# Kernel optimization log

Measured on AMD Instinct MI355X. Metric: run time of the kernel, lower is better.

The kernel has to match this reference:

```python
import jax, jax.numpy as jnp
import numpy as np

B, N, D = 8, 2048, 1024  # batch, seq_len, input_dim (= dim_k = dim_v)

def setup_inputs() -> dict:
    key = jax.random.key(0)
    k1, k2, k3, k4, k5 = jax.random.split(key, 5)
    s = 1.0 / np.sqrt(D)
    return {
        "img": jax.random.normal(k1, (B, N, D), dtype=jnp.float32),
        "text": jax.random.normal(k2, (B, N, D), dtype=jnp.float32),
        "Wq": jax.random.normal(k3, (D, D), dtype=jnp.float32) * s,
        "Wk": jax.random.normal(k4, (D, D), dtype=jnp.float32) * s,
        "Wv": jax.random.normal(k5, (D, D), dtype=jnp.float32) * s,
    }

def reference(img, text, Wq, Wk, Wv):
    # Linear layers (bias=False): y = x @ W^T (torch Linear convention)
    Q = jnp.einsum('bnd,kd->bnk', img, Wq)    # [B, N, dim_k]
    K = jnp.einsum('bmd,kd->bmk', text, Wk)   # [B, M, dim_k]
    V = jnp.einsum('bmd,vd->bmv', text, Wv)   # [B, M, dim_v]
    alpha_qk = jnp.einsum('bnk,bmk->bnm', Q, K)  # QK^T, no 1/sqrt(dk) scaling (as in source)
    alpha = jax.nn.softmax(alpha_qk, axis=1)     # softmax over QUERY axis (dim=1), as in source
    out = jnp.einsum('bnm,bmv->bnv', alpha, V)   # [B, N, dim_v]
    feature = out + text
    return (out, feature)
```

## Files before the change

### kernel.cpp

```cpp
#include <hip/hip_runtime.h>
#include <math.h>

#define B 8
#define N 2048
#define D 1024

#define BM 128
#define BN 128
#define BK 32

typedef __bf16 bf16;
typedef __bf16 bf16x8 __attribute__((ext_vector_type(8)));
typedef __bf16 bf16x4 __attribute__((ext_vector_type(4)));
typedef float f32x4 __attribute__((ext_vector_type(4)));

__device__ __forceinline__ void load_lds16(const void* g, void* l) {
    __builtin_amdgcn_global_load_lds((const __attribute__((address_space(1))) void*)g,
                                     (__attribute__((address_space(3))) void*)l, 16, 0, 0);
}

#define MFMA16(a, b, c) __builtin_amdgcn_mfma_f32_16x16x32_bf16(a, b, c, 0, 0, 0)
#define BARRIER() asm volatile("s_barrier" ::: "memory")
#define WAITV0() asm volatile("s_waitcnt vmcnt(0)" ::: "memory")

__global__ __launch_bounds__(256) void split_fp32(const float* __restrict__ x,
                                                  bf16* __restrict__ h,
                                                  bf16* __restrict__ l, long n)
{
    long i = ((long)blockIdx.x * 256 + threadIdx.x) * 4;
    if (i >= n) return;
    float4 v = *(const float4*)(x + i);
    float vs[4] = {v.x, v.y, v.z, v.w};
    bf16x4 hh, ll;
#pragma unroll
    for (int t = 0; t < 4; ++t) {
        bf16 hv = (bf16)vs[t];
        hh[t] = hv;
        ll[t] = (bf16)(vs[t] - (float)hv);
    }
    *(bf16x4*)(h + i) = hh;
    *(bf16x4*)(l + i) = ll;
}

__global__ __launch_bounds__(256) void tsplit_1024(const float* __restrict__ W,
                                                   bf16* __restrict__ WT_h,
                                                   bf16* __restrict__ WT_l)
{
    __shared__ float tile[64][65];
    const int d0 = blockIdx.x * 64, k0 = blockIdx.y * 64;
    const int tx = threadIdx.x & 63, ty = threadIdx.x >> 6;
#pragma unroll
    for (int r = 0; r < 16; ++r) {
        int kl = ty + r * 4;
        tile[kl][tx] = W[(size_t)(k0 + kl) * 1024 + d0 + tx];
    }
    __syncthreads();
#pragma unroll
    for (int r = 0; r < 16; ++r) {
        int dl = ty + r * 4;
        float v = tile[tx][dl];
        bf16 hv = (bf16)v;
        size_t idx = (size_t)(d0 + dl) * 1024 + k0 + tx;
        WT_h[idx] = hv;
        WT_l[idx] = (bf16)(v - (float)hv);
    }
}

template<int TERMS, int EPI>
__global__ __launch_bounds__(256) void gemm_nt_mfma(
    const bf16* __restrict__ Ah_g, const bf16* __restrict__ Al_g,
    const bf16* __restrict__ Bh_g, const bf16* __restrict__ Bl_g,
    bf16* __restrict__ Chi, bf16* __restrict__ Clo,
    float* __restrict__ Cf, const float* __restrict__ Text,
    float* __restrict__ Feat,
    int Mdim, int Ncdim, int Kdim, long sA, long sB, long sC)
{
    __shared__ bf16 Ah[BM][BK];
    __shared__ bf16 Bh[BN][BK];
    __shared__ bf16 Al[BM][BK];
    __shared__ bf16 Bl[BN][BK];

    const int tid = threadIdx.x;
    const int lane = tid & 63;
    const int wv = tid >> 6;
    const int wr = (wv >> 1) * 64;
    const int wc = (wv & 1) * 64;
    const int mfrag = lane & 15;
    const int quad = lane >> 4;

    const long z = blockIdx.z;
    const int row0 = blockIdx.y * BM;
    const int col0 = blockIdx.x * BN;

    const bf16* Abh = Ah_g + z * sA;
    const bf16* Abl = (TERMS == 3) ? (Al_g + z * sA) : nullptr;
    const bf16* Bbh = Bh_g + z * sB;
    const bf16* Bbl = (TERMS == 3) ? (Bl_g + z * sB) : nullptr;

    f32x4 acc[4][4] = {};

    for (int k0 = 0; k0 < Kdim; k0 += BK) {
#pragma unroll
        for (int q = 0; q < 2; ++q) {
            int c = q * 256 + tid;
            int row = c >> 2, kp = (c & 3) * 8;
            load_lds16(Abh + (long)(row0 + row) * Kdim + k0 + kp, &Ah[row][kp]);
            load_lds16(Bbh + (long)(col0 + row) * Kdim + k0 + kp, &Bh[row][kp]);
            if constexpr (TERMS == 3) {
                load_lds16(Abl + (long)(row0 + row) * Kdim + k0 + kp, &Al[row][kp]);
                load_lds16(Bbl + (long)(col0 + row) * Kdim + k0 + kp, &Bl[row][kp]);
            }
        }
        __syncthreads();

        bf16x8 a_h[4], b_h[4], a_l[4], b_l[4];
#pragma unroll
        for (int i = 0; i < 4; ++i) {
            a_h[i] = *(const bf16x8*)&Ah[wr + i * 16 + mfrag][quad * 8];
            b_h[i] = *(const bf16x8*)&Bh[wc + i * 16 + mfrag][quad * 8];
            if constexpr (TERMS == 3) {
                a_l[i] = *(const bf16x8*)&Al[wr + i * 16 + mfrag][quad * 8];
                b_l[i] = *(const bf16x8*)&Bl[wc + i * 16 + mfrag][quad * 8];
            }
        }
#pragma unroll
        for (int i = 0; i < 4; ++i)
#pragma unroll
            for (int j = 0; j < 4; ++j) {
                acc[i][j] = MFMA16(a_h[i], b_h[j], acc[i][j]);
                if constexpr (TERMS == 3) {
                    acc[i][j] = MFMA16(a_h[i], b_l[j], acc[i][j]);
                    acc[i][j] = MFMA16(a_l[i], b_h[j], acc[i][j]);
                }
            }
        __syncthreads();
    }

    const long cbase = z * sC;
    const bool wlo = (Clo != nullptr);
#pragma unroll
    for (int i = 0; i < 4; ++i) {
#pragma unroll
        for (int r = 0; r < 4; ++r) {
            int row = row0 + wr + i * 16 + quad * 4 + r;
#pragma unroll
            for (int j = 0; j < 4; ++j) {
                int col = col0 + wc + j * 16 + mfrag;
                long idx = cbase + (long)row * Ncdim + col;
                float v = acc[i][j][r];
                if constexpr (EPI == 0) {
                    bf16 h = (bf16)v;
                    Chi[idx] = h;
                    if (wlo) Clo[idx] = (bf16)(v - (float)h);
                } else if constexpr (EPI == 1) {
                    Cf[idx] = v;
                } else {
                    Cf[idx] = v;
                    Feat[idx] = v + Text[idx];
                }
            }
        }
    }
}


__device__ __forceinline__ void xcd_swz(int& bx, int& by, int gx, int gy) {
    int nwg = gx * gy;
    int flat = by * gx + bx;
    flat = (flat & 7) * (nwg >> 3) + (flat >> 3);
    bx = flat % gx;
    by = flat / gx;
}

__device__ __forceinline__ void stage32(const bf16* __restrict__ g, int Kd, int k0,
                                        bf16* l, int tid)
{
#pragma unroll
    for (int c = 0; c < 2; ++c) {
        int idx = c * 512 + tid;
        int row = idx >> 2;
        int slot = idx & 3;
        int kk = ((slot ^ ((row >> 1) & 3)) << 3);
        load_lds16(g + (long)row * Kd + k0 + kk, l + (size_t)idx * 8);
    }
}

__device__ __forceinline__ void stage64(const bf16* __restrict__ g, int Kd, int k0,
                                        bf16* l, int tid)
{
#pragma unroll
    for (int c = 0; c < 4; ++c) {
        int idx = c * 512 + tid;
        int row = idx >> 3;
        int slot = idx & 7;
        int kk = ((slot ^ (row & 7)) << 3);
        load_lds16(g + (long)row * Kd + k0 + kk, l + (size_t)idx * 8);
    }
}

__device__ __forceinline__ bf16x8 rd32(const bf16* l, int row, int quad) {
    return *(const bf16x8*)(l + row * 32 + ((quad ^ ((row >> 1) & 3)) << 3));
}
__device__ __forceinline__ bf16x8 rd64(const bf16* l, int row, int ks, int quad) {
    return *(const bf16x8*)(l + row * 64 + (((ks * 4 + quad) ^ (row & 7)) << 3));
}

template<int EPI>
__global__ __launch_bounds__(512) void gemm256_3t(
    const bf16* __restrict__ Ah_g, const bf16* __restrict__ Al_g,
    const bf16* __restrict__ Bh_g, const bf16* __restrict__ Bl_g,
    bf16* __restrict__ Chi, bf16* __restrict__ Clo, float* __restrict__ Cf,
    int Ncdim, int Kdim, long sA, long sB, long sC)
{
    __shared__ __align__(16) bf16 lds[2][4][256 * 32];

    const int tid = threadIdx.x;
    const int lane = tid & 63;
    const int wv = tid >> 6;
    const int wrow = (wv >> 2) << 7;
    const int wcol = (wv & 3) << 6;
    const int mfrag = lane & 15;
    const int quad = lane >> 4;

    const long z = blockIdx.z;
    int bx = blockIdx.x, by = blockIdx.y;
    xcd_swz(bx, by, gridDim.x, gridDim.y);
    const int row0 = by * 256;
    const int col0 = bx * 256;

    const bf16* Abh = Ah_g + z * sA + (long)row0 * Kdim;
    const bf16* Abl = Al_g + z * sA + (long)row0 * Kdim;
    const bf16* Bbh = Bh_g + z * sB + (long)col0 * Kdim;
    const bf16* Bbl = Bl_g + z * sB + (long)col0 * Kdim;

    f32x4 acc[8][4] = {};
    const int NT = Kdim >> 5;

    stage32(Abh, Kdim, 0, lds[0][0], tid);
    stage32(Bbh, Kdim, 0, lds[0][2], tid);
    stage32(Abl, Kdim, 0, lds[0][1], tid);
    stage32(Bbl, Kdim, 0, lds[0][3], tid);

    for (int t = 0; t < NT; ++t) {
        const int cur = t & 1;
        const bf16* LAh = lds[cur][0];
        const bf16* LAl = lds[cur][1];
        const bf16* LBh = lds[cur][2];
        const bf16* LBl = lds[cur][3];
        const bool pf = (t + 1 < NT);
        const int kn = (t + 1) << 5;

        WAITV0();
        BARRIER();

        bf16x8 ah[8], bh[4], bl[4], al[8];
#pragma unroll
        for (int i = 0; i < 8; ++i) ah[i] = rd32(LAh, wrow + i * 16 + mfrag, quad);
#pragma unroll
        for (int j = 0; j < 4; ++j) bh[j] = rd32(LBh, wcol + j * 16 + mfrag, quad);

        __builtin_amdgcn_s_setprio(1);
#pragma unroll
        for (int i = 0; i < 4; ++i)
#pragma unroll
            for (int j = 0; j < 4; ++j)
                acc[i][j] = MFMA16(ah[i], bh[j], acc[i][j]);
        __builtin_amdgcn_s_setprio(0);

        if (pf) { stage32(Abh, Kdim, kn, lds[cur ^ 1][0], tid);
                  stage32(Bbh, Kdim, kn, lds[cur ^ 1][2], tid); }

#pragma unroll
        for (int j = 0; j < 4; ++j) bl[j] = rd32(LBl, wcol + j * 16 + mfrag, quad);

        __builtin_amdgcn_s_setprio(1);
#pragma unroll
        for (int i = 4; i < 8; ++i)
#pragma unroll
            for (int j = 0; j < 4; ++j)
                acc[i][j] = MFMA16(ah[i], bh[j], acc[i][j]);
        __builtin_amdgcn_s_setprio(0);

#pragma unroll
        for (int i = 0; i < 4; ++i) al[i] = rd32(LAl, wrow + i * 16 + mfrag, quad);

        __builtin_amdgcn_s_setprio(1);
#pragma unroll
        for (int i = 0; i < 4; ++i)
#pragma unroll
            for (int j = 0; j < 4; ++j)
                acc[i][j] = MFMA16(ah[i], bl[j], acc[i][j]);
        __builtin_amdgcn_s_setprio(0);

        if (pf) { stage32(Abl, Kdim, kn, lds[cur ^ 1][1], tid);
                  stage32(Bbl, Kdim, kn, lds[cur ^ 1][3], tid); }

#pragma unroll
        for (int i = 4; i < 8; ++i) al[i] = rd32(LAl, wrow + i * 16 + mfrag, quad);

        __builtin_amdgcn_s_setprio(1);
#pragma unroll
        for (int i = 4; i < 8; ++i)
#pragma unroll
            for (int j = 0; j < 4; ++j)
                acc[i][j] = MFMA16(ah[i], bl[j], acc[i][j]);

#pragma unroll
        for (int i = 0; i < 8; ++i)
#pragma unroll
            for (int j = 0; j < 4; ++j)
                acc[i][j] = MFMA16(al[i], bh[j], acc[i][j]);
        __builtin_amdgcn_s_setprio(0);
    }

    const long cbase = z * sC;
    const bool wlo = (Clo != nullptr);
#pragma unroll
    for (int i = 0; i < 8; ++i) {
#pragma unroll
        for (int r = 0; r < 4; ++r) {
            int row = row0 + wrow + i * 16 + quad * 4 + r;
            long rbase = cbase + (long)row * Ncdim;
#pragma unroll
            for (int j = 0; j < 4; ++j) {
                int col = col0 + wcol + j * 16 + mfrag;
                float v = acc[i][j][r];
                if constexpr (EPI == 0) {
                    bf16 h = (bf16)v;
                    Chi[rbase + col] = h;
                    if (wlo) Clo[rbase + col] = (bf16)(v - (float)h);
                } else {
                    Cf[rbase + col] = v;
                }
            }
        }
    }
}

template<int EPI>
__global__ __launch_bounds__(512) void gemm256_1t(
    const bf16* __restrict__ A_g, const bf16* __restrict__ B_g,
    bf16* __restrict__ Chi, float* __restrict__ Cf,
    const float* __restrict__ Text, float* __restrict__ Feat,
    int Ncdim, int Kdim, long sA, long sB, long sC)
{
    __shared__ __align__(16) bf16 lds[2][2][256 * 64];

    const int tid = threadIdx.x;
    const int lane = tid & 63;
    const int wv = tid >> 6;
    const int wrow = (wv >> 2) << 7;
    const int wcol = (wv & 3) << 6;
    const int mfrag = lane & 15;
    const int quad = lane >> 4;

    const long z = blockIdx.z;
    int bx = blockIdx.x, by = blockIdx.y;
    xcd_swz(bx, by, gridDim.x, gridDim.y);
    const int row0 = by * 256;
    const int col0 = bx * 256;

    const bf16* Ab = A_g + z * sA + (long)row0 * Kdim;
    const bf16* Bb = B_g + z * sB + (long)col0 * Kdim;

    f32x4 acc[8][4] = {};
    const int NT = Kdim >> 6;

    stage64(Ab, Kdim, 0, lds[0][0], tid);
    stage64(Bb, Kdim, 0, lds[0][1], tid);

    for (int t = 0; t < NT; ++t) {
        const int cur = t & 1;
        const bf16* LA = lds[cur][0];
        const bf16* LB = lds[cur][1];
        const bool pf = (t + 1 < NT);
        const int kn = (t + 1) << 6;

        WAITV0();
        BARRIER();

        bf16x8 a[8][2], b[4][2];
#pragma unroll
        for (int i = 0; i < 4; ++i)
#pragma unroll
            for (int ks = 0; ks < 2; ++ks)
                a[i][ks] = rd64(LA, wrow + i * 16 + mfrag, ks, quad);
#pragma unroll
        for (int j = 0; j < 2; ++j)
#pragma unroll
            for (int ks = 0; ks < 2; ++ks)
                b[j][ks] = rd64(LB, wcol + j * 16 + mfrag, ks, quad);

        __builtin_amdgcn_s_setprio(1);
#pragma unroll
        for (int i = 0; i < 4; ++i)
#pragma unroll
            for (int j = 0; j < 2; ++j)
#pragma unroll
                for (int ks = 0; ks < 2; ++ks)
                    acc[i][j] = MFMA16(a[i][ks], b[j][ks], acc[i][j]);
        __builtin_amdgcn_s_setprio(0);

        if (pf) stage64(Ab, Kdim, kn, lds[cur ^ 1][0], tid);

#pragma unroll
        for (int j = 2; j < 4; ++j)
#pragma unroll
            for (int ks = 0; ks < 2; ++ks)
                b[j][ks] = rd64(LB, wcol + j * 16 + mfrag, ks, quad);

        __builtin_amdgcn_s_setprio(1);
#pragma unroll
        for (int i = 0; i < 4; ++i)
#pragma unroll
            for (int j = 2; j < 4; ++j)
#pragma unroll
                for (int ks = 0; ks < 2; ++ks)
                    acc[i][j] = MFMA16(a[i][ks], b[j][ks], acc[i][j]);
        __builtin_amdgcn_s_setprio(0);

#pragma unroll
        for (int i = 4; i < 8; ++i)
#pragma unroll
            for (int ks = 0; ks < 2; ++ks)
                a[i][ks] = rd64(LA, wrow + i * 16 + mfrag, ks, quad);

        __builtin_amdgcn_s_setprio(1);
#pragma unroll
        for (int i = 4; i < 8; ++i)
#pragma unroll
            for (int j = 2; j < 4; ++j)
#pragma unroll
                for (int ks = 0; ks < 2; ++ks)
                    acc[i][j] = MFMA16(a[i][ks], b[j][ks], acc[i][j]);
        __builtin_amdgcn_s_setprio(0);

        if (pf) stage64(Bb, Kdim, kn, lds[cur ^ 1][1], tid);

        __builtin_amdgcn_s_setprio(1);
#pragma unroll
        for (int i = 4; i < 8; ++i)
#pragma unroll
            for (int j = 0; j < 2; ++j)
#pragma unroll
                for (int ks = 0; ks < 2; ++ks)
                    acc[i][j] = MFMA16(a[i][ks], b[j][ks], acc[i][j]);
        __builtin_amdgcn_s_setprio(0);
    }

    const long cbase = z * sC;
#pragma unroll
    for (int i = 0; i < 8; ++i) {
#pragma unroll
        for (int r = 0; r < 4; ++r) {
            int row = row0 + wrow + i * 16 + quad * 4 + r;
            long rbase = cbase + (long)row * Ncdim;
#pragma unroll
            for (int j = 0; j < 4; ++j) {
                int col = col0 + wcol + j * 16 + mfrag;
                float v = acc[i][j][r];
                if constexpr (EPI == 0) {
                    Chi[rbase + col] = (bf16)v;
                } else {
                    Cf[rbase + col] = v;
                    Feat[rbase + col] = v + Text[rbase + col];
                }
            }
        }
    }
}

__global__ __launch_bounds__(1024) void col_softmax_bf16(const float* __restrict__ S,
                                                         bf16* __restrict__ Aout)
{
    const int b = blockIdx.x / (N / 64);
    const int mbase = (blockIdx.x % (N / 64)) * 64;
    const int t = threadIdx.x;
    const int mloc = t & 63;
    const int slice = t >> 6;
    const int m = mbase + mloc;
    const float* Sb = S + (size_t)b * N * N;
    bf16* Ab = Aout + (size_t)b * N * N;
    const int n_lo = slice * (N / 16), n_hi = n_lo + (N / 16);

    __shared__ float red_m[16][64];
    __shared__ float red_s[16][64];

    float mx = -INFINITY, s = 0.0f;
    for (int n = n_lo; n < n_hi; n += 8) {
        float x[8];
#pragma unroll
        for (int u = 0; u < 8; ++u) x[u] = Sb[(size_t)(n + u) * N + m];
        float bm = x[0];
#pragma unroll
        for (int u = 1; u < 8; ++u) bm = fmaxf(bm, x[u]);
        float nm = fmaxf(mx, bm);
        float a = 0.0f;
#pragma unroll
        for (int u = 0; u < 8; ++u) a += __expf(x[u] - nm);
        s = s * __expf(mx - nm) + a;
        mx = nm;
    }
    red_m[slice][mloc] = mx;
    red_s[slice][mloc] = s;
    __syncthreads();

    float gm = -INFINITY;
#pragma unroll
    for (int i = 0; i < 16; ++i) gm = fmaxf(gm, red_m[i][mloc]);
    float den = 0.0f;
#pragma unroll
    for (int i = 0; i < 16; ++i) den += red_s[i][mloc] * __expf(red_m[i][mloc] - gm);
    float inv = 1.0f / den;

    for (int n = n_lo; n < n_hi; n += 8) {
        float x[8];
#pragma unroll
        for (int u = 0; u < 8; ++u) x[u] = Sb[(size_t)(n + u) * N + m];
#pragma unroll
        for (int u = 0; u < 8; ++u)
            Ab[(size_t)(n + u) * N + m] = (bf16)(__expf(x[u] - gm) * inv);
    }
}

extern "C" void kernel_launch(void* const* d_in, const int* in_sizes, int n_in,
                              void* d_out, int out_size, void* d_ws, size_t ws_size,
                              hipStream_t stream)
{
    const float* img  = (const float*)d_in[0];
    const float* text = (const float*)d_in[1];
    const float* Wq   = (const float*)d_in[2];
    const float* Wk   = (const float*)d_in[3];
    const float* Wv   = (const float*)d_in[4];

    const long E  = (long)B * N * D;
    const long W2 = (long)D * D;
    const long EN = (long)B * N * N;

    char* ws = (char*)d_ws;
    float* S     = (float*)ws;
    bf16* img_h  = (bf16*)ws;
    bf16* img_l  = img_h + E;
    bf16* WqT_h  = (bf16*)(ws + (size_t)4 * E);
    bf16* WqT_l  = WqT_h + W2;
    bf16* WkT_h  = WqT_l + W2;
    bf16* WkT_l  = WkT_h + W2;
    bf16* Wqk_h  = WkT_l + W2;
    bf16* Wqk_l  = Wqk_h + W2;
    bf16* Wv_l_s = Wqk_l + W2;
    float* out_pv = (float*)ws;

    bf16* text_h = (bf16*)(ws + (size_t)EN * 4);
    bf16* text_l = text_h + E;
    bf16* VT_h   = text_l;

    bf16* T_h  = (bf16*)d_out;
    bf16* T_l  = T_h + E;
    bf16* Wv_h = T_l + E;
    bf16* alpha = (bf16*)d_out;
    float* out  = (float*)d_out;
    float* feat = out + E;

    dim3 blk(256);
    dim3 blk5(512);

    split_fp32<<<E / 1024, blk, 0, stream>>>(img,  img_h,  img_l,  E);
    split_fp32<<<E / 1024, blk, 0, stream>>>(text, text_h, text_l, E);
    split_fp32<<<W2 / 1024, blk, 0, stream>>>(Wv, Wv_h, Wv_l_s, W2);
    tsplit_1024<<<dim3(16, 16), blk, 0, stream>>>(Wq, WqT_h, WqT_l);
    tsplit_1024<<<dim3(16, 16), blk, 0, stream>>>(Wk, WkT_h, WkT_l);

    gemm_nt_mfma<3, 0><<<dim3(8, 8, 1), blk, 0, stream>>>(
        WkT_h, WkT_l, WqT_h, WqT_l, Wqk_h, Wqk_l, nullptr, nullptr, nullptr,
        D, D, D, 0, 0, 0);

    gemm256_3t<0><<<dim3(D / 256, (B * N) / 256, 1), blk5, 0, stream>>>(
        img_h, img_l, Wqk_h, Wqk_l, T_h, T_l, nullptr,
        D, D, 0, 0, 0);

    gemm256_3t<1><<<dim3(N / 256, N / 256, B), blk5, 0, stream>>>(
        T_h, T_l, text_h, text_l, nullptr, nullptr, S,
        N, D, (long)N * D, (long)N * D, (long)N * N);

    gemm256_1t<0><<<dim3(N / 256, D / 256, B), blk5, 0, stream>>>(
        Wv_h, text_h, VT_h, nullptr, nullptr, nullptr,
        N, D, 0, (long)N * D, (long)D * N);

    col_softmax_bf16<<<dim3(B * N / 64), dim3(1024), 0, stream>>>(S, alpha);

    gemm256_1t<2><<<dim3(D / 256, N / 256, B), blk5, 0, stream>>>(
        alpha, VT_h, nullptr, out_pv, text, feat,
        D, N, (long)N * N, (long)D * N, (long)N * D);

    hipMemcpyAsync(out, out_pv, (size_t)E * 4, hipMemcpyDeviceToDevice, stream);
}
```

Before: 738.0 us.

## Switch 256x256 GEMM kernels to 32x32x16 MFMA with pointer-increment staging

Replaces the 16x16x32 bf16 MFMA tiles in both the 3-term split GEMM and the single-term GEMM with 32x32x16 MFMA tiles. This halves the MFMA instruction count and cuts LDS fragment reads per output. Global-to-LDS staging now uses precomputed swizzled offsets and pointers advanced each k-step instead of recomputing addresses. The LDS read pattern and the epilogue row mapping are rewritten to match the 32x32 accumulator layout, and the larger 16-float accumulators change register pressure and the store pattern.

```diff
diff --git a/kernel.cpp b/kernel.cpp
--- a/kernel.cpp
+++ b/kernel.cpp
@@ -13,6 +13,7 @@
 typedef __bf16 bf16x8 __attribute__((ext_vector_type(8)));
 typedef __bf16 bf16x4 __attribute__((ext_vector_type(4)));
 typedef float f32x4 __attribute__((ext_vector_type(4)));
+typedef float f32x16 __attribute__((ext_vector_type(16)));
 
 __device__ __forceinline__ void load_lds16(const void* g, void* l) {
     __builtin_amdgcn_global_load_lds((const __attribute__((address_space(1))) void*)g,
@@ -20,6 +21,7 @@
 }
 
 #define MFMA16(a, b, c) __builtin_amdgcn_mfma_f32_16x16x32_bf16(a, b, c, 0, 0, 0)
+#define MFMA32(a, b, c) __builtin_amdgcn_mfma_f32_32x32x16_bf16(a, b, c, 0, 0, 0)
 #define BARRIER() asm volatile("s_barrier" ::: "memory")
 #define WAITV0() asm volatile("s_waitcnt vmcnt(0)" ::: "memory")
 
@@ -172,39 +174,6 @@
     by = flat / gx;
 }
 
-__device__ __forceinline__ void stage32(const bf16* __restrict__ g, int Kd, int k0,
-                                        bf16* l, int tid)
-{
-#pragma unroll
-    for (int c = 0; c < 2; ++c) {
-        int idx = c * 512 + tid;
-        int row = idx >> 2;
-        int slot = idx & 3;
-        int kk = ((slot ^ ((row >> 1) & 3)) << 3);
-        load_lds16(g + (long)row * Kd + k0 + kk, l + (size_t)idx * 8);
-    }
-}
-
-__device__ __forceinline__ void stage64(const bf16* __restrict__ g, int Kd, int k0,
-                                        bf16* l, int tid)
-{
-#pragma unroll
-    for (int c = 0; c < 4; ++c) {
-        int idx = c * 512 + tid;
-        int row = idx >> 3;
-        int slot = idx & 7;
-        int kk = ((slot ^ (row & 7)) << 3);
-        load_lds16(g + (long)row * Kd + k0 + kk, l + (size_t)idx * 8);
-    }
-}
-
-__device__ __forceinline__ bf16x8 rd32(const bf16* l, int row, int quad) {
-    return *(const bf16x8*)(l + row * 32 + ((quad ^ ((row >> 1) & 3)) << 3));
-}
-__device__ __forceinline__ bf16x8 rd64(const bf16* l, int row, int ks, int quad) {
-    return *(const bf16x8*)(l + row * 64 + (((ks * 4 + quad) ^ (row & 7)) << 3));
-}
-
 template<int EPI>
 __global__ __launch_bounds__(512) void gemm256_3t(
     const bf16* __restrict__ Ah_g, const bf16* __restrict__ Al_g,
@@ -219,8 +188,9 @@
     const int wv = tid >> 6;
     const int wrow = (wv >> 2) << 7;
     const int wcol = (wv & 3) << 6;
-    const int mfrag = lane & 15;
-    const int quad = lane >> 4;
+    const int rl = lane & 31;
+    const int hi = lane >> 5;
+    const int sx = (lane >> 1) & 3;
 
     const long z = blockIdx.z;
     int bx = blockIdx.x, by = blockIdx.y;
@@ -228,18 +198,32 @@
     const int row0 = by * 256;
     const int col0 = bx * 256;
 
-    const bf16* Abh = Ah_g + z * sA + (long)row0 * Kdim;
-    const bf16* Abl = Al_g + z * sA + (long)row0 * Kdim;
-    const bf16* Bbh = Bh_g + z * sB + (long)col0 * Kdim;
-    const bf16* Bbl = Bl_g + z * sB + (long)col0 * Kdim;
-
-    f32x4 acc[8][4] = {};
+    const int sr0 = tid >> 2;
+    const long soff0 = (long)sr0 * Kdim + (((tid & 3) ^ ((sr0 >> 1) & 3)) << 3);
+    const long soff1 = soff0 + ((long)Kdim << 7);
+
+    const bf16* pAh = Ah_g + z * sA + (long)row0 * Kdim;
+    const bf16* pAl = Al_g + z * sA + (long)row0 * Kdim;
+    const bf16* pBh = Bh_g + z * sB + (long)col0 * Kdim;
+    const bf16* pBl = Bl_g + z * sB + (long)col0 * Kdim;
+
+    const int rdA0 = (wrow + rl) * 32;
+    const int rdB0 = (wcol + rl) * 32;
+    const int s0 = (hi ^ sx) << 3;
+    const int s1 = ((2 + hi) ^ sx) << 3;
+
+    f32x16 acc[4][2] = {};
     const int NT = Kdim >> 5;
 
-    stage32(Abh, Kdim, 0, lds[0][0], tid);
-    stage32(Bbh, Kdim, 0, lds[0][2], tid);
-    stage32(Abl, Kdim, 0, lds[0][1], tid);
-    stage32(Bbl, Kdim, 0, lds[0][3], tid);
+    load_lds16(pAh + soff0, &lds[0][0][tid * 8]);
+    load_lds16(pAh + soff1, &lds[0][0][4096 + tid * 8]);
+    load_lds16(pBh + soff0, &lds[0][2][tid * 8]);
+    load_lds16(pBh + soff1, &lds[0][2][4096 + tid * 8]);
+    load_lds16(pAl + soff0, &lds[0][1][tid * 8]);
+    load_lds16(pAl + soff1, &lds[0][1][4096 + tid * 8]);
+    load_lds16(pBl + soff0, &lds[0][3][tid * 8]);
+    load_lds16(pBl + soff1, &lds[0][3][4096 + tid * 8]);
+    pAh += 32; pAl += 32; pBh += 32; pBl += 32;
 
     for (int t = 0; t < NT; ++t) {
         const int cur = t & 1;
@@ -247,90 +231,137 @@
         const bf16* LAl = lds[cur][1];
         const bf16* LBh = lds[cur][2];
         const bf16* LBl = lds[cur][3];
+        bf16* SAh = lds[cur ^ 1][0];
+        bf16* SAl = lds[cur ^ 1][1];
+        bf16* SBh = lds[cur ^ 1][2];
+        bf16* SBl = lds[cur ^ 1][3];
         const bool pf = (t + 1 < NT);
-        const int kn = (t + 1) << 5;
 
         WAITV0();
         BARRIER();
 
-        bf16x8 ah[8], bh[4], bl[4], al[8];
-#pragma unroll
-        for (int i = 0; i < 8; ++i) ah[i] = rd32(LAh, wrow + i * 16 + mfrag, quad);
-#pragma unroll
-        for (int j = 0; j < 4; ++j) bh[j] = rd32(LBh, wcol + j * 16 + mfrag, quad);
+        bf16x8 ah[4][2], bh[2][2], bl[2][2], al[2][2];
+#pragma unroll
+        for (int i = 0; i < 4; ++i) {
+            ah[i][0] = *(const bf16x8*)(LAh + rdA0 + i * 1024 + s0);
+            ah[i][1] = *(const bf16x8*)(LAh + rdA0 + i * 1024 + s1);
+        }
+#pragma unroll
+        for (int j = 0; j < 2; ++j) {
+            bh[j][0] = *(const bf16x8*)(LBh + rdB0 + j * 1024 + s0);
+            bh[j][1] = *(const bf16x8*)(LBh + rdB0 + j * 1024 + s1);
+        }
 
         __builtin_amdgcn_s_setprio(1);
 #pragma unroll
-        for (int i = 0; i < 4; ++i)
-#pragma unroll
-            for (int j = 0; j < 4; ++j)
-                acc[i][j] = MFMA16(ah[i], bh[j], acc[i][j]);
+        for (int i = 0; i < 2; ++i)
+#pragma unroll
+            for (int j = 0; j < 2; ++j)
+#pragma unroll
+                for (int ks = 0; ks < 2; ++ks)
+                    acc[i][j] = MFMA32(ah[i][ks], bh[j][ks], acc[i][j]);
         __builtin_amdgcn_s_setprio(0);
 
-        if (pf) { stage32(Abh, Kdim, kn, lds[cur ^ 1][0], tid);
-                  stage32(Bbh, Kdim, kn, lds[cur ^ 1][2], tid); }
-
-#pragma unroll
-        for (int j = 0; j < 4; ++j) bl[j] = rd32(LBl, wcol + j * 16 + mfrag, quad);
+        if (pf) {
+            load_lds16(pAh + soff0, SAh + tid * 8);
+            load_lds16(pAh + soff1, SAh + 4096 + tid * 8);
+            load_lds16(pBh + soff0, SBh + tid * 8);
+            load_lds16(pBh + soff1, SBh + 4096 + tid * 8);
+        }
+
+#pragma unroll
+        for (int j = 0; j < 2; ++j) {
+            bl[j][0] = *(const bf16x8*)(LBl + rdB0 + j * 1024 + s0);
+            bl[j][1] = *(const bf16x8*)(LBl + rdB0 + j * 1024 + s1);
+        }
 
         __builtin_amdgcn_s_setprio(1);
 #pragma unroll
-        for (int i = 4; i < 8; ++i)
-#pragma unroll
-            for (int j = 0; j < 4; ++j)
-                acc[i][j] = MFMA16(ah[i], bh[j], acc[i][j]);
+        for (int i = 0; i < 2; ++i)
+#pragma unroll
+            for (int j = 0; j < 2; ++j)
+#pragma unroll
+                for (int ks = 0; ks < 2; ++ks)
+                    acc[2 + i][j] = MFMA32(ah[2 + i][ks], bh[j][ks], acc[2 + i][j]);
         __builtin_amdgcn_s_setprio(0);
 
 #pragma unroll
-        for (int i = 0; i < 4; ++i) al[i] = rd32(LAl, wrow + i * 16 + mfrag, quad);
+        for (int i = 0; i < 2; ++i) {
+            al[i][0] = *(const bf16x8*)(LAl + rdA0 + i * 1024 + s0);
+            al[i][1] = *(const bf16x8*)(LAl + rdA0 + i * 1024 + s1);
+        }
 
         __builtin_amdgcn_s_setprio(1);
 #pragma unroll
-        for (int i = 0; i < 4; ++i)
-#pragma unroll
-            for (int j = 0; j < 4; ++j)
-                acc[i][j] = MFMA16(ah[i], bl[j], acc[i][j]);
+        for (int i = 0; i < 2; ++i)
+#pragma unroll
+            for (int j = 0; j < 2; ++j)
+#pragma unroll
+                for (int ks = 0; ks < 2; ++ks)
+                    acc[i][j] = MFMA32(ah[i][ks], bl[j][ks], acc[i][j]);
         __builtin_amdgcn_s_setprio(0);
 
-        if (pf) { stage32(Abl, Kdim, kn, lds[cur ^ 1][1], tid);
-                  stage32(Bbl, Kdim, kn, lds[cur ^ 1][3], tid); }
-
-#pragma unroll
-        for (int i = 4; i < 8; ++i) al[i] = rd32(LAl, wrow + i * 16 + mfrag, quad);
+        if (pf) {
+            load_lds16(pAl + soff0, SAl + tid * 8);
+            load_lds16(pAl + soff1, SAl + 4096 + tid * 8);
+            load_lds16(pBl + soff0, SBl + tid * 8);
+            load_lds16(pBl + soff1, SBl + 4096 + tid * 8);
+        }
 
         __builtin_amdgcn_s_setprio(1);
 #pragma unroll
-        for (int i = 4; i < 8; ++i)
-#pragma unroll
-            for (int j = 0; j < 4; ++j)
-                acc[i][j] = MFMA16(ah[i], bl[j], acc[i][j]);
-
-#pragma unroll
-        for (int i = 0; i < 8; ++i)
-#pragma unroll
-            for (int j = 0; j < 4; ++j)
-                acc[i][j] = MFMA16(al[i], bh[j], acc[i][j]);
+        for (int i = 0; i < 2; ++i)
+#pragma unroll
+            for (int j = 0; j < 2; ++j)
+#pragma unroll
+                for (int ks = 0; ks < 2; ++ks)
+                    acc[i][j] = MFMA32(al[i][ks], bh[j][ks], acc[i][j]);
         __builtin_amdgcn_s_setprio(0);
+
+#pragma unroll
+        for (int i = 0; i < 2; ++i) {
+            al[i][0] = *(const bf16x8*)(LAl + rdA0 + (2 + i) * 1024 + s0);
+            al[i][1] = *(const bf16x8*)(LAl + rdA0 + (2 + i) * 1024 + s1);
+        }
+
+        __builtin_amdgcn_s_setprio(1);
+#pragma unroll
+        for (int i = 0; i < 2; ++i)
+#pragma unroll
+            for (int j = 0; j < 2; ++j)
+#pragma unroll
+                for (int ks = 0; ks < 2; ++ks)
+                    acc[2 + i][j] = MFMA32(ah[2 + i][ks], bl[j][ks], acc[2 + i][j]);
+#pragma unroll
+        for (int i = 0; i < 2; ++i)
+#pragma unroll
+            for (int j = 0; j < 2; ++j)
+#pragma unroll
+                for (int ks = 0; ks < 2; ++ks)
+                    acc[2 + i][j] = MFMA32(al[i][ks], bh[j][ks], acc[2 + i][j]);
+        __builtin_amdgcn_s_setprio(0);
+
+        pAh += 32; pAl += 32; pBh += 32; pBl += 32;
     }
 
     const long cbase = z * sC;
     const bool wlo = (Clo != nullptr);
 #pragma unroll
-    for (int i = 0; i < 8; ++i) {
-#pragma unroll
-        for (int r = 0; r < 4; ++r) {
-            int row = row0 + wrow + i * 16 + quad * 4 + r;
-            long rbase = cbase + (long)row * Ncdim;
-#pragma unroll
-            for (int j = 0; j < 4; ++j) {
-                int col = col0 + wcol + j * 16 + mfrag;
+    for (int i = 0; i < 4; ++i) {
+#pragma unroll
+        for (int j = 0; j < 2; ++j) {
+            int col = col0 + wcol + j * 32 + rl;
+#pragma unroll
+            for (int r = 0; r < 16; ++r) {
+                int row = row0 + wrow + i * 32 + (r & 3) + ((r >> 2) << 3) + (hi << 2);
+                long idx = cbase + (long)row * Ncdim + col;
                 float v = acc[i][j][r];
                 if constexpr (EPI == 0) {
                     bf16 h = (bf16)v;
-                    Chi[rbase + col] = h;
-                    if (wlo) Clo[rbase + col] = (bf16)(v - (float)h);
+                    Chi[idx] = h;
+                    if (wlo) Clo[idx] = (bf16)(v - (float)h);
                 } else {
-                    Cf[rbase + col] = v;
+                    Cf[idx] = v;
                 }
             }
         }
@@ -351,8 +382,9 @@
     const int wv = tid >> 6;
     const int wrow = (wv >> 2) << 7;
     const int wcol = (wv & 3) << 6;
-    const int mfrag = lane & 15;
-    const int quad = lane >> 4;
+    const int rl = lane & 31;
+    const int hi = lane >> 5;
+    const int sx8 = lane & 7;
 
     const long z = blockIdx.z;
     int bx = blockIdx.x, by = blockIdx.y;
@@ -360,110 +392,108 @@
     const int row0 = by * 256;
     const int col0 = bx * 256;
 
-    const bf16* Ab = A_g + z * sA + (long)row0 * Kdim;
-    const bf16* Bb = B_g + z * sB + (long)col0 * Kdim;
-
-    f32x4 acc[8][4] = {};
+    const long soffS = (long)(tid >> 3) * Kdim + ((((tid & 7) ^ ((tid >> 3) & 7))) << 3);
+    const long sstep = (long)Kdim << 6;
+
+    const bf16* pA = A_g + z * sA + (long)row0 * Kdim;
+    const bf16* pB = B_g + z * sB + (long)col0 * Kdim;
+
+    const int rdA0 = (wrow + rl) * 64;
+    const int rdB0 = (wcol + rl) * 64;
+    int sl[4];
+#pragma unroll
+    for (int ks = 0; ks < 4; ++ks) sl[ks] = ((ks * 2 + hi) ^ sx8) << 3;
+
+    f32x16 acc[4][2] = {};
     const int NT = Kdim >> 6;
 
-    stage64(Ab, Kdim, 0, lds[0][0], tid);
-    stage64(Bb, Kdim, 0, lds[0][1], tid);
+#pragma unroll
+    for (int c = 0; c < 4; ++c) {
+        load_lds16(pA + soffS + c * sstep, &lds[0][0][c * 4096 + tid * 8]);
+        load_lds16(pB + soffS + c * sstep, &lds[0][1][c * 4096 + tid * 8]);
+    }
+    pA += 64; pB += 64;
 
     for (int t = 0; t < NT; ++t) {
         const int cur = t & 1;
         const bf16* LA = lds[cur][0];
         const bf16* LB = lds[cur][1];
+        bf16* SA = lds[cur ^ 1][0];
+        bf16* SB = lds[cur ^ 1][1];
         const bool pf = (t + 1 < NT);
-        const int kn = (t + 1) << 6;
 
         WAITV0();
         BARRIER();
 
-        bf16x8 a[8][2], b[4][2];
-#pragma unroll
-        for (int i = 0; i < 4; ++i)
-#pragma unroll
-            for (int ks = 0; ks < 2; ++ks)
-                a[i][ks] = rd64(LA, wrow + i * 16 + mfrag, ks, quad);
+        bf16x8 a[2][4], b[2][4];
+#pragma unroll
+        for (int ii = 0; ii < 2; ++ii)
+#pragma unroll
+            for (int ks = 0; ks < 4; ++ks)
+                a[ii][ks] = *(const bf16x8*)(LA + rdA0 + ii * 2048 + sl[ks]);
 #pragma unroll
         for (int j = 0; j < 2; ++j)
 #pragma unroll
-            for (int ks = 0; ks < 2; ++ks)
-                b[j][ks] = rd64(LB, wcol + j * 16 + mfrag, ks, quad);
+            for (int ks = 0; ks < 4; ++ks)
+                b[j][ks] = *(const bf16x8*)(LB + rdB0 + j * 2048 + sl[ks]);
 
         __builtin_amdgcn_s_setprio(1);
 #pragma unroll
-        for (int i = 0; i < 4; ++i)
-#pragma unroll
-            for (int j = 0; j < 2; ++j)
-#pragma unroll
-                for (int ks = 0; ks < 2; ++ks)
-                    acc[i][j] = MFMA16(a[i][ks], b[j][ks], acc[i][j]);
+        for (int ii = 0; ii < 2; ++ii)
+#pragma unroll
+            for (int j = 0; j < 2; ++j)
+#pragma unroll
+                for (int ks = 0; ks < 4; ++ks)
+                    acc[ii][j] = MFMA32(a[ii][ks], b[j][ks], acc[ii][j]);
         __builtin_amdgcn_s_setprio(0);
 
-        if (pf) stage64(Ab, Kdim, kn, lds[cur ^ 1][0], tid);
-
-#pragma unroll
-        for (int j = 2; j < 4; ++j)
-#pragma unroll
-            for (int ks = 0; ks < 2; ++ks)
-                b[j][ks] = rd64(LB, wcol + j * 16 + mfrag, ks, quad);
+        if (pf) {
+#pragma unroll
+            for (int c = 0; c < 4; ++c)
+                load_lds16(pA + soffS + c * sstep, SA + c * 4096 + tid * 8);
+        }
+
+#pragma unroll
+        for (int ii = 0; ii < 2; ++ii)
+#pragma unroll
+            for (int ks = 0; ks < 4; ++ks)
+                a[ii][ks] = *(const bf16x8*)(LA + rdA0 + (2 + ii) * 2048 + sl[ks]);
 
         __builtin_amdgcn_s_setprio(1);
 #pragma unroll
-        for (int i = 0; i < 4; ++i)
-#pragma unroll
-            for (int j = 2; j < 4; ++j)
-#pragma unroll
-                for (int ks = 0; ks < 2; ++ks)
-                    acc[i][j] = MFMA16(a[i][ks], b[j][ks], acc[i][j]);
+        for (int ii = 0; ii < 2; ++ii)
+#pragma unroll
+            for (int j = 0; j < 2; ++j)
+#pragma unroll
+                for (int ks = 0; ks < 4; ++ks)
+                    acc[2 + ii][j] = MFMA32(a[ii][ks], b[j][ks], acc[2 + ii][j]);
         __builtin_amdgcn_s_setprio(0);
 
-#pragma unroll
-        for (int i = 4; i < 8; ++i)
-#pragma unroll
-            for (int ks = 0; ks < 2; ++ks)
-                a[i][ks] = rd64(LA, wrow + i * 16 + mfrag, ks, quad);
-
-        __builtin_amdgcn_s_setprio(1);
-#pragma unroll
-        for (int i = 4; i < 8; ++i)
-#pragma unroll
-            for (int j = 2; j < 4; ++j)
-#pragma unroll
-                for (int ks = 0; ks < 2; ++ks)
-                    acc[i][j] = MFMA16(a[i][ks], b[j][ks], acc[i][j]);
-        __builtin_amdgcn_s_setprio(0);
-
-        if (pf) stage64(Bb, Kdim, kn, lds[cur ^ 1][1], tid);
-
-        __builtin_amdgcn_s_setprio(1);
-#pragma unroll
-        for (int i = 4; i < 8; ++i)
-#pragma unroll
-            for (int j = 0; j < 2; ++j)
-#pragma unroll
-                for (int ks = 0; ks < 2; ++ks)
-                    acc[i][j] = MFMA16(a[i][ks], b[j][ks], acc[i][j]);
-        __builtin_amdgcn_s_setprio(0);
+        if (pf) {
+#pragma unroll
+            for (int c = 0; c < 4; ++c)
+                load_lds16(pB + soffS + c * sstep, SB + c * 4096 + tid * 8);
+        }
+
+        pA += 64; pB += 64;
     }
 
     const long cbase = z * sC;
 #pragma unroll
-    for (int i = 0; i < 8; ++i) {
-#pragma unroll
-        for (int r = 0; r < 4; ++r) {
-            int row = row0 + wrow + i * 16 + quad * 4 + r;
-            long rbase = cbase + (long)row * Ncdim;
-#pragma unroll
-            for (int j = 0; j < 4; ++j) {
-                int col = col0 + wcol + j * 16 + mfrag;
+    for (int i = 0; i < 4; ++i) {
+#pragma unroll
+        for (int j = 0; j < 2; ++j) {
+            int col = col0 + wcol + j * 32 + rl;
+#pragma unroll
+            for (int r = 0; r < 16; ++r) {
+                int row = row0 + wrow + i * 32 + (r & 3) + ((r >> 2) << 3) + (hi << 2);
+                long idx = cbase + (long)row * Ncdim + col;
                 float v = acc[i][j][r];
                 if constexpr (EPI == 0) {
-                    Chi[rbase + col] = (bf16)v;
+                    Chi[idx] = (bf16)v;
                 } else {
-                    Cf[rbase + col] = v;
-                    Feat[rbase + col] = v + Text[rbase + col];
+                    Cf[idx] = v;
+                    Feat[idx] = v + Text[idx];
                 }
             }
         }
```

Result: slower. 790.0 us (+7.0%).

## Software-pipeline 3-term GEMM, fuse split launches, use 128-tile GEMM for projection

Applied to the files above, without the earlier changes.

Restructures the bf16x3 GEMM main loop so the al*bh MFMA block of each K tile is deferred into the next iteration, using ping-pong register buffers. This lets that block overlap the next tile's LDS reads, and the wait now covers both vmcnt and lgkmcnt. The img and text fp32 splits are merged into one launch. The img@Wqk projection moves from the 256-tile kernel to the 128-tile gemm_nt_mfma kernel, which gives a larger grid. The extra live register buffers raise register pressure, and the loop unrolled by two assumes NT is even.

```diff
diff --git a/kernel.cpp b/kernel.cpp
--- a/kernel.cpp
+++ b/kernel.cpp
@@ -22,6 +22,7 @@
 #define MFMA16(a, b, c) __builtin_amdgcn_mfma_f32_16x16x32_bf16(a, b, c, 0, 0, 0)
 #define BARRIER() asm volatile("s_barrier" ::: "memory")
 #define WAITV0() asm volatile("s_waitcnt vmcnt(0)" ::: "memory")
+#define WAITALL() asm volatile("s_waitcnt vmcnt(0) lgkmcnt(0)" ::: "memory")
 
 __global__ __launch_bounds__(256) void split_fp32(const float* __restrict__ x,
                                                   bf16* __restrict__ h,
@@ -29,6 +30,30 @@
 {
     long i = ((long)blockIdx.x * 256 + threadIdx.x) * 4;
     if (i >= n) return;
+    float4 v = *(const float4*)(x + i);
+    float vs[4] = {v.x, v.y, v.z, v.w};
+    bf16x4 hh, ll;
+#pragma unroll
+    for (int t = 0; t < 4; ++t) {
+        bf16 hv = (bf16)vs[t];
+        hh[t] = hv;
+        ll[t] = (bf16)(vs[t] - (float)hv);
+    }
+    *(bf16x4*)(h + i) = hh;
+    *(bf16x4*)(l + i) = ll;
+}
+
+__global__ __launch_bounds__(256) void split_fp32_x2(
+    const float* __restrict__ x0, bf16* __restrict__ h0, bf16* __restrict__ l0,
+    const float* __restrict__ x1, bf16* __restrict__ h1, bf16* __restrict__ l1,
+    long n)
+{
+    long nb = n / 1024;
+    long bid = blockIdx.x;
+    const float* x; bf16 *h, *l;
+    if (bid < nb) { x = x0; h = h0; l = l0; }
+    else { x = x1; h = h1; l = l1; bid -= nb; }
+    long i = (bid * 256 + threadIdx.x) * 4;
     float4 v = *(const float4*)(x + i);
     float vs[4] = {v.x, v.y, v.z, v.w};
     bf16x4 hh, ll;
@@ -205,6 +230,58 @@
     return *(const bf16x8*)(l + row * 64 + (((ks * 4 + quad) ^ (row & 7)) << 3));
 }
 
+
+#define TILE_BODY(T, CUR, ALP, BHP, ALF, BHF, DOPEND)                         \
+  {                                                                           \
+    const bf16* LAh = lds[CUR][0]; const bf16* LAl = lds[CUR][1];             \
+    const bf16* LBh = lds[CUR][2]; const bf16* LBl = lds[CUR][3];             \
+    bf16* SAh = lds[CUR ^ 1][0]; bf16* SAl = lds[CUR ^ 1][1];                 \
+    bf16* SBh = lds[CUR ^ 1][2]; bf16* SBl = lds[CUR ^ 1][3];                 \
+    const bool pf = ((T) + 1 < NT);                                           \
+    const int kn = ((T) + 1) << 5;                                            \
+    WAITALL();                                                                \
+    BARRIER();                                                                \
+    _Pragma("unroll") for (int i = 0; i < 8; ++i)                             \
+        ah[i] = rd32(LAh, wrow + i * 16 + mfrag, quad);                       \
+    _Pragma("unroll") for (int j = 0; j < 4; ++j)                             \
+        BHF[j] = rd32(LBh, wcol + j * 16 + mfrag, quad);                      \
+    if (DOPEND) {                                                             \
+        __builtin_amdgcn_s_setprio(1);                                        \
+        _Pragma("unroll") for (int i = 0; i < 8; ++i)                         \
+        _Pragma("unroll") for (int j = 0; j < 4; ++j)                         \
+            acc[i][j] = MFMA16(ALP[i], BHP[j], acc[i][j]);                    \
+        __builtin_amdgcn_s_setprio(0);                                        \
+    }                                                                         \
+    if (pf) { stage32(Abh, Kdim, kn, SAh, tid);                               \
+              stage32(Bbh, Kdim, kn, SBh, tid); }                             \
+    __builtin_amdgcn_s_setprio(1);                                            \
+    _Pragma("unroll") for (int i = 0; i < 4; ++i)                             \
+    _Pragma("unroll") for (int j = 0; j < 4; ++j)                             \
+        acc[i][j] = MFMA16(ah[i], BHF[j], acc[i][j]);                         \
+    __builtin_amdgcn_s_setprio(0);                                            \
+    _Pragma("unroll") for (int j = 0; j < 4; ++j)                             \
+        bl[j] = rd32(LBl, wcol + j * 16 + mfrag, quad);                       \
+    __builtin_amdgcn_s_setprio(1);                                            \
+    _Pragma("unroll") for (int i = 4; i < 8; ++i)                             \
+    _Pragma("unroll") for (int j = 0; j < 4; ++j)                             \
+        acc[i][j] = MFMA16(ah[i], BHF[j], acc[i][j]);                         \
+    __builtin_amdgcn_s_setprio(0);                                            \
+    _Pragma("unroll") for (int i = 0; i < 8; ++i)                             \
+        ALF[i] = rd32(LAl, wrow + i * 16 + mfrag, quad);                      \
+    __builtin_amdgcn_s_setprio(1);                                            \
+    _Pragma("unroll") for (int i = 0; i < 4; ++i)                             \
+    _Pragma("unroll") for (int j = 0; j < 4; ++j)                             \
+        acc[i][j] = MFMA16(ah[i], bl[j], acc[i][j]);                          \
+    __builtin_amdgcn_s_setprio(0);                                            \
+    if (pf) { stage32(Abl, Kdim, kn, SAl, tid);                               \
+              stage32(Bbl, Kdim, kn, SBl, tid); }                             \
+    __builtin_amdgcn_s_setprio(1);                                            \
+    _Pragma("unroll") for (int i = 4; i < 8; ++i)                             \
+    _Pragma("unroll") for (int j = 0; j < 4; ++j)                             \
+        acc[i][j] = MFMA16(ah[i], bl[j], acc[i][j]);                          \
+    __builtin_amdgcn_s_setprio(0);                                            \
+  }
+
 template<int EPI>
 __global__ __launch_bounds__(512) void gemm256_3t(
     const bf16* __restrict__ Ah_g, const bf16* __restrict__ Al_g,
@@ -241,77 +318,22 @@
     stage32(Abl, Kdim, 0, lds[0][1], tid);
     stage32(Bbl, Kdim, 0, lds[0][3], tid);
 
-    for (int t = 0; t < NT; ++t) {
-        const int cur = t & 1;
-        const bf16* LAh = lds[cur][0];
-        const bf16* LAl = lds[cur][1];
-        const bf16* LBh = lds[cur][2];
-        const bf16* LBl = lds[cur][3];
-        const bool pf = (t + 1 < NT);
-        const int kn = (t + 1) << 5;
-
-        WAITV0();
-        BARRIER();
-
-        bf16x8 ah[8], bh[4], bl[4], al[8];
-#pragma unroll
-        for (int i = 0; i < 8; ++i) ah[i] = rd32(LAh, wrow + i * 16 + mfrag, quad);
-#pragma unroll
-        for (int j = 0; j < 4; ++j) bh[j] = rd32(LBh, wcol + j * 16 + mfrag, quad);
-
-        __builtin_amdgcn_s_setprio(1);
-#pragma unroll
-        for (int i = 0; i < 4; ++i)
-#pragma unroll
-            for (int j = 0; j < 4; ++j)
-                acc[i][j] = MFMA16(ah[i], bh[j], acc[i][j]);
-        __builtin_amdgcn_s_setprio(0);
-
-        if (pf) { stage32(Abh, Kdim, kn, lds[cur ^ 1][0], tid);
-                  stage32(Bbh, Kdim, kn, lds[cur ^ 1][2], tid); }
-
-#pragma unroll
-        for (int j = 0; j < 4; ++j) bl[j] = rd32(LBl, wcol + j * 16 + mfrag, quad);
-
-        __builtin_amdgcn_s_setprio(1);
-#pragma unroll
-        for (int i = 4; i < 8; ++i)
-#pragma unroll
-            for (int j = 0; j < 4; ++j)
-                acc[i][j] = MFMA16(ah[i], bh[j], acc[i][j]);
-        __builtin_amdgcn_s_setprio(0);
-
-#pragma unroll
-        for (int i = 0; i < 4; ++i) al[i] = rd32(LAl, wrow + i * 16 + mfrag, quad);
-
-        __builtin_amdgcn_s_setprio(1);
-#pragma unroll
-        for (int i = 0; i < 4; ++i)
-#pragma unroll
-            for (int j = 0; j < 4; ++j)
-                acc[i][j] = MFMA16(ah[i], bl[j], acc[i][j]);
-        __builtin_amdgcn_s_setprio(0);
-
-        if (pf) { stage32(Abl, Kdim, kn, lds[cur ^ 1][1], tid);
-                  stage32(Bbl, Kdim, kn, lds[cur ^ 1][3], tid); }
-
-#pragma unroll
-        for (int i = 4; i < 8; ++i) al[i] = rd32(LAl, wrow + i * 16 + mfrag, quad);
-
-        __builtin_amdgcn_s_setprio(1);
-#pragma unroll
-        for (int i = 4; i < 8; ++i)
-#pragma unroll
-            for (int j = 0; j < 4; ++j)
-                acc[i][j] = MFMA16(ah[i], bl[j], acc[i][j]);
-
-#pragma unroll
-        for (int i = 0; i < 8; ++i)
-#pragma unroll
-            for (int j = 0; j < 4; ++j)
-                acc[i][j] = MFMA16(al[i], bh[j], acc[i][j]);
-        __builtin_amdgcn_s_setprio(0);
-    }
+    bf16x8 ah[8], bl[4];
+    bf16x8 bhA[4], bhB[4], alA[8], alB[8];
+
+    TILE_BODY(0, 0, alB, bhB, alA, bhA, false);
+    TILE_BODY(1, 1, alA, bhA, alB, bhB, true);
+    for (int t = 2; t < NT; t += 2) {
+        TILE_BODY(t, 0, alB, bhB, alA, bhA, true);
+        TILE_BODY(t + 1, 1, alA, bhA, alB, bhB, true);
+    }
+    __builtin_amdgcn_s_setprio(1);
+#pragma unroll
+    for (int i = 0; i < 8; ++i)
+#pragma unroll
+        for (int j = 0; j < 4; ++j)
+            acc[i][j] = MFMA16(alB[i], bhB[j], acc[i][j]);
+    __builtin_amdgcn_s_setprio(0);
 
     const long cbase = z * sC;
     const bool wlo = (Clo != nullptr);
@@ -373,6 +395,8 @@
         const int cur = t & 1;
         const bf16* LA = lds[cur][0];
         const bf16* LB = lds[cur][1];
+        bf16* SA = lds[cur ^ 1][0];
+        bf16* SB = lds[cur ^ 1][1];
         const bool pf = (t + 1 < NT);
         const int kn = (t + 1) << 6;
 
@@ -401,7 +425,7 @@
                     acc[i][j] = MFMA16(a[i][ks], b[j][ks], acc[i][j]);
         __builtin_amdgcn_s_setprio(0);
 
-        if (pf) stage64(Ab, Kdim, kn, lds[cur ^ 1][0], tid);
+        if (pf) stage64(Ab, Kdim, kn, SA, tid);
 
 #pragma unroll
         for (int j = 2; j < 4; ++j)
@@ -435,7 +459,7 @@
                     acc[i][j] = MFMA16(a[i][ks], b[j][ks], acc[i][j]);
         __builtin_amdgcn_s_setprio(0);
 
-        if (pf) stage64(Bb, Kdim, kn, lds[cur ^ 1][1], tid);
+        if (pf) stage64(Bb, Kdim, kn, SB, tid);
 
         __builtin_amdgcn_s_setprio(1);
 #pragma unroll
@@ -564,8 +588,8 @@
     dim3 blk(256);
     dim3 blk5(512);
 
-    split_fp32<<<E / 1024, blk, 0, stream>>>(img,  img_h,  img_l,  E);
-    split_fp32<<<E / 1024, blk, 0, stream>>>(text, text_h, text_l, E);
+    split_fp32_x2<<<2 * (E / 1024), blk, 0, stream>>>(
+        img, img_h, img_l, text, text_h, text_l, E);
     split_fp32<<<W2 / 1024, blk, 0, stream>>>(Wv, Wv_h, Wv_l_s, W2);
     tsplit_1024<<<dim3(16, 16), blk, 0, stream>>>(Wq, WqT_h, WqT_l);
     tsplit_1024<<<dim3(16, 16), blk, 0, stream>>>(Wk, WkT_h, WkT_l);
@@ -574,9 +598,9 @@
         WkT_h, WkT_l, WqT_h, WqT_l, Wqk_h, Wqk_l, nullptr, nullptr, nullptr,
         D, D, D, 0, 0, 0);
 
-    gemm256_3t<0><<<dim3(D / 256, (B * N) / 256, 1), blk5, 0, stream>>>(
-        img_h, img_l, Wqk_h, Wqk_l, T_h, T_l, nullptr,
-        D, D, 0, 0, 0);
+    gemm_nt_mfma<3, 0><<<dim3(D / BN, (B * N) / BM, 1), blk, 0, stream>>>(
+        img_h, img_l, Wqk_h, Wqk_l, T_h, T_l, nullptr, nullptr, nullptr,
+        B * N, D, D, 0, 0, 0);
 
     gemm256_3t<1><<<dim3(N / 256, N / 256, B), blk5, 0, stream>>>(
         T_h, T_l, text_h, text_l, nullptr, nullptr, S,
```

After: 1.003 ms. 1.36x slower.
